# Kernel optimization log

Measured on AMD Instinct MI355X. Metric: run time of the kernel, lower is better.

The kernel has to match this reference:

```python
import jax, jax.numpy as jnp
import numpy as np

EMBED_DIM = 768
HEAD_SIZE = 64

def setup_inputs() -> dict:
    key = jax.random.key(0)
    k1, k2, k3, k4 = jax.random.split(key, 4)
    x = jax.random.normal(k1, (4, 4096, EMBED_DIM), dtype=jnp.float32)
    # nn.Linear(E, H, bias=False) weights, stored as [E, H] for y = x @ W
    scale = 1.0 / np.sqrt(EMBED_DIM)
    Wk = jax.random.uniform(k2, (EMBED_DIM, HEAD_SIZE), jnp.float32, -scale, scale)
    Wq = jax.random.uniform(k3, (EMBED_DIM, HEAD_SIZE), jnp.float32, -scale, scale)
    Wv = jax.random.uniform(k4, (EMBED_DIM, HEAD_SIZE), jnp.float32, -scale, scale)
    return {"x": x, "Wk": Wk, "Wq": Wq, "Wv": Wv}

def reference(x, Wk, Wq, Wv):
    # x: [B, S, E]
    E = x.shape[2]
    K = jnp.einsum("bse,eh->bsh", x, Wk)  # [B, S, H]
    Q = jnp.einsum("bse,eh->bsh", x, Wq)
    V = jnp.einsum("bse,eh->bsh", x, Wv)
    # NOTE: original scales by embedding_dim**0.5, not head_size**0.5
    A = jnp.einsum("bqh,bkh->bqk", Q, K) / jnp.sqrt(jnp.asarray(E, x.dtype))
    A = jax.nn.softmax(A, axis=-1)
    # dropout is inference-mode identity
    return jnp.einsum("bqk,bkh->bqh", A, V)
```

## Files before the change

### kernel.cpp

```cpp
#include <hip/hip_runtime.h>

typedef __attribute__((ext_vector_type(8))) short short8;
typedef __attribute__((ext_vector_type(4))) short short4v;
typedef __attribute__((ext_vector_type(4))) float float4v;
typedef __attribute__((ext_vector_type(2))) int int2v;

__device__ __forceinline__ short f2bf(float f) {
    union { float f; unsigned u; } v; v.f = f;
    return (short)((v.u + 0x7fffu + ((v.u >> 16) & 1u)) >> 16);
}
__device__ __forceinline__ int pack2(float a, float b) {
    union { float f; unsigned u; } x, y; x.f = a; y.f = b;
    return (int)(((x.u + 0x8000u) >> 16) | ((y.u + 0x8000u) & 0xFFFF0000u));
}

__device__ __forceinline__ float fast_exp2(float x) {
#if __has_builtin(__builtin_amdgcn_exp2f)
    return __builtin_amdgcn_exp2f(x);
#else
    return exp2f(x);
#endif
}

__global__ void wtrans_kernel(const float* __restrict__ Wk, const float* __restrict__ Wq,
                              const float* __restrict__ Wv, short* __restrict__ Wt3T) {
    int idx = blockIdx.x * 256 + threadIdx.x;
    int p = idx / 12288;
    int rem = idx - p * 12288;
    int kstep = rem / 512;
    int r2 = rem - kstep * 512;
    int lane = r2 >> 3, i = r2 & 7;
    int quad = lane >> 4, l16 = lane & 15;
    int j = p >> 2, nt = p & 3;
    int n = nt * 16 + l16;
    int k = kstep * 32 + quad * 8 + i;
    const float* W = (j == 0) ? Wq : (j == 1 ? Wk : Wv);
    float scale = (j == 0) ? 0.05205877f : 1.0f;
    Wt3T[idx] = f2bf(W[k * 64 + n] * scale);
}

__global__ __launch_bounds__(256, 3) void proj_kernel(
    const float* __restrict__ x, const short* __restrict__ Wt3T,
    short* __restrict__ Qs, short* __restrict__ Kb, short* __restrict__ Vtr)
{
    __shared__ alignas(16) short As[24 * 512];
    const int tid = threadIdx.x;
    const int wave = tid >> 6, lane = tid & 63, quad = lane >> 4, l16 = lane & 15;
    const int m0 = blockIdx.x * 16;
    const int p0 = wave * 3;

    {
        const int r = tid >> 4, c16 = tid & 15;
        const float* xp = x + (size_t)(m0 + r) * 768 + c16 * 4;
        float4 v[12];
#pragma unroll
        for (int ch = 0; ch < 12; ++ch) v[ch] = *(const float4*)(xp + ch * 64);
#pragma unroll
        for (int ch = 0; ch < 12; ++ch) {
            const int cb = c16 * 4 + ch * 64;
            const int sidx = (cb >> 5) * 512 + ((((cb >> 3) & 3) * 16 + r) << 3) + (cb & 7);
            *(int2v*)&As[sidx] = (int2v){pack2(v[ch].x, v[ch].y), pack2(v[ch].z, v[ch].w)};
        }
    }
    __syncthreads();

    const short* wp0 = Wt3T + (size_t)(p0 + 0) * 12288 + lane * 8;
    const short* wp1 = Wt3T + (size_t)(p0 + 1) * 12288 + lane * 8;
    const short* wp2 = Wt3T + (size_t)(p0 + 2) * 12288 + lane * 8;

    float4v acc0 = (float4v){0.f, 0.f, 0.f, 0.f};
    float4v acc1 = acc0, acc2 = acc0;

#pragma unroll
    for (int it = 0; it < 24; ++it) {
        short8 a = *(const short8*)&As[it * 512 + lane * 8];
        short8 w0 = *(const short8*)(wp0 + it * 512);
        short8 w1 = *(const short8*)(wp1 + it * 512);
        short8 w2 = *(const short8*)(wp2 + it * 512);
        acc0 = __builtin_amdgcn_mfma_f32_16x16x32_bf16(a, w0, acc0, 0, 0, 0);
        acc1 = __builtin_amdgcn_mfma_f32_16x16x32_bf16(a, w1, acc1, 0, 0, 0);
        acc2 = __builtin_amdgcn_mfma_f32_16x16x32_bf16(a, w2, acc2, 0, 0, 0);
    }

    float4v accs[3] = {acc0, acc1, acc2};
#pragma unroll
    for (int t = 0; t < 3; ++t) {
        const int p = p0 + t, j = p >> 2, nt = p & 3;
        if (j < 2) {
            short* dst = (j == 0) ? Qs : Kb;
#pragma unroll
            for (int r = 0; r < 4; ++r)
                dst[(size_t)(m0 + quad * 4 + r) * 64 + nt * 16 + l16] = f2bf(accs[t][r]);
        }
    }
    __syncthreads();
    short* sm = As;
#pragma unroll
    for (int t = 0; t < 3; ++t) {
        const int p = p0 + t, nt = p & 3;
        if ((p >> 2) == 2)
#pragma unroll
            for (int r = 0; r < 4; ++r)
                sm[(quad * 4 + r) * 72 + nt * 16 + l16] = f2bf(accs[t][r]);
    }
    __syncthreads();
    {
        const int h = tid >> 2, si = (tid & 3) * 4;
        const int b = m0 >> 12, s0 = m0 & 4095;
        short4v tmp;
#pragma unroll
        for (int i = 0; i < 4; ++i) tmp[i] = sm[(si + i) * 72 + h];
        *(short4v*)(Vtr + (size_t)(b * 64 + h) * 4096 + s0 + si) = tmp;
    }
}

__global__ __launch_bounds__(256, 4) void attn_kernel(
    const short* __restrict__ Qs, const short* __restrict__ Kb, const short* __restrict__ Vt,
    float* __restrict__ out, float* __restrict__ Lsum, int kv_len)
{
    __shared__ alignas(16) short Kl[64 * 72];
    __shared__ alignas(16) short Vl[64 * 72];
    __shared__ alignas(16) short Pl[4 * 32 * 72];

    const int tid = threadIdx.x;
    const int wave = tid >> 6, lane = tid & 63, quad = lane >> 4, l16 = lane & 15;
    const int qt = blockIdx.x, b = blockIdx.y, sp = blockIdx.z;
    const int q0 = qt * 128;
    const int bS = b * 4096;
    const int kv0 = sp * kv_len;

    short8 qa[2][2];
#pragma unroll
    for (int mt = 0; mt < 2; ++mt)
#pragma unroll
        for (int ks = 0; ks < 2; ++ks)
            qa[mt][ks] = *(const short8*)(Qs + (size_t)(bS + q0 + wave * 32 + mt * 16 + l16) * 64 + ks * 32 + quad * 8);

    float4v o[2][4];
    float rs[2][4];
#pragma unroll
    for (int mt = 0; mt < 2; ++mt)
#pragma unroll
        for (int nt = 0; nt < 4; ++nt) o[mt][nt] = (float4v){0.f, 0.f, 0.f, 0.f};
#pragma unroll
    for (int mt = 0; mt < 2; ++mt)
#pragma unroll
        for (int r = 0; r < 4; ++r) rs[mt][r] = 0.f;

    const int sr = tid >> 2, sc = (tid & 3) * 16;
    short* plw = &Pl[wave * 2304];

    for (int kt = 0; kt < kv_len; kt += 64) {
        const int kvg = kv0 + kt;
        __syncthreads();
        {
            const short* src = Kb + (size_t)(bS + kvg + sr) * 64 + sc;
            *(short8*)&Kl[sr * 72 + sc]     = *(const short8*)src;
            *(short8*)&Kl[sr * 72 + sc + 8] = *(const short8*)(src + 8);
            const short* vs = Vt + (size_t)(b * 64 + sr) * 4096 + kvg + sc;
            *(short8*)&Vl[sr * 72 + sc]     = *(const short8*)vs;
            *(short8*)&Vl[sr * 72 + sc + 8] = *(const short8*)(vs + 8);
        }
        __syncthreads();

        float4v s[2][4];
#pragma unroll
        for (int nt = 0; nt < 4; ++nt) {
            short8 b0 = *(const short8*)&Kl[(nt * 16 + l16) * 72 + quad * 8];
            short8 b1 = *(const short8*)&Kl[(nt * 16 + l16) * 72 + 32 + quad * 8];
#pragma unroll
            for (int mt = 0; mt < 2; ++mt) {
                float4v a0 = (float4v){0.f, 0.f, 0.f, 0.f};
                a0 = __builtin_amdgcn_mfma_f32_16x16x32_bf16(qa[mt][0], b0, a0, 0, 0, 0);
                a0 = __builtin_amdgcn_mfma_f32_16x16x32_bf16(qa[mt][1], b1, a0, 0, 0, 0);
                s[mt][nt] = a0;
            }
        }

#pragma unroll
        for (int mt = 0; mt < 2; ++mt)
#pragma unroll
            for (int nt = 0; nt < 4; ++nt)
#pragma unroll
                for (int r = 0; r < 4; ++r) {
                    float p = fast_exp2(s[mt][nt][r]);
                    rs[mt][r] += p;
                    plw[(mt * 16 + quad * 4 + r) * 72 + nt * 16 + l16] =
                        (short)((__float_as_uint(p) + 0x8000u) >> 16);
                }

#pragma unroll
        for (int ks = 0; ks < 2; ++ks) {
            short8 bf[4];
#pragma unroll
            for (int nt = 0; nt < 4; ++nt)
                bf[nt] = *(const short8*)&Vl[(nt * 16 + l16) * 72 + ks * 32 + quad * 8];
#pragma unroll
            for (int mt = 0; mt < 2; ++mt) {
                short8 af = *(const short8*)&plw[(mt * 16 + l16) * 72 + ks * 32 + quad * 8];
#pragma unroll
                for (int nt = 0; nt < 4; ++nt)
                    o[mt][nt] = __builtin_amdgcn_mfma_f32_16x16x32_bf16(af, bf[nt], o[mt][nt], 0, 0, 0);
            }
        }
    }

#pragma unroll
    for (int mt = 0; mt < 2; ++mt)
#pragma unroll
        for (int r = 0; r < 4; ++r) {
#pragma unroll
            for (int off = 8; off >= 1; off >>= 1)
                rs[mt][r] += __shfl_xor(rs[mt][r], off);
        }

#pragma unroll
    for (int mt = 0; mt < 2; ++mt) {
#pragma unroll
        for (int nt = 0; nt < 4; ++nt)
#pragma unroll
            for (int r = 0; r < 4; ++r) {
                int qb = q0 + wave * 32 + mt * 16 + quad * 4 + r;
                atomicAdd(&out[(size_t)(bS + qb) * 64 + nt * 16 + l16], o[mt][nt][r]);
            }
        if (l16 == 0) {
#pragma unroll
            for (int r = 0; r < 4; ++r) {
                int qb = q0 + wave * 32 + mt * 16 + quad * 4 + r;
                atomicAdd(&Lsum[bS + qb], rs[mt][r]);
            }
        }
    }
}

__global__ void normalize_kernel(float* __restrict__ out, const float* __restrict__ Lsum) {
    int idx = blockIdx.x * 256 + threadIdx.x;
    out[idx] /= Lsum[idx >> 6];
}

extern "C" void kernel_launch(void* const* d_in, const int* in_sizes, int n_in,
                              void* d_out, int out_size, void* d_ws, size_t ws_size,
                              hipStream_t stream) {
    const float* x  = (const float*)d_in[0];
    const float* Wk = (const float*)d_in[1];
    const float* Wq = (const float*)d_in[2];
    const float* Wv = (const float*)d_in[3];
    float* out = (float*)d_out;

    char* w = (char*)d_ws;
    size_t off = 0;
    auto take = [&](size_t bytes) -> void* {
        void* p = w + off;
        off = (off + bytes + 255) & ~(size_t)255;
        return p;
    };
    short* Qs   = (short*)take((size_t)16384 * 64 * 2);
    short* Kb   = (short*)take((size_t)16384 * 64 * 2);
    short* Vt   = (short*)take((size_t)16384 * 64 * 2);
    short* Wt3  = (short*)take((size_t)3 * 64 * 768 * 2);
    float* Lsum = (float*)take((size_t)16384 * 4);

    hipMemsetAsync(out, 0, (size_t)out_size * sizeof(float), stream);
    hipMemsetAsync(Lsum, 0, (size_t)16384 * 4, stream);

    wtrans_kernel<<<576, 256, 0, stream>>>(Wk, Wq, Wv, Wt3);
    proj_kernel<<<1024, 256, 0, stream>>>(x, Wt3, Qs, Kb, Vt);
    const int nsplit = 8;
    dim3 ag(32, 4, nsplit);
    attn_kernel<<<ag, 256, 0, stream>>>(Qs, Kb, Vt, out, Lsum, 4096 / nsplit);
    normalize_kernel<<<4096, 256, 0, stream>>>(out, Lsum);
}
```

Before: 153.0 us.

## Prefetch K/V tiles into registers and transpose QK MFMA for packed P stores

Global loads of the next K/V tile are issued into registers right after the LDS barrier, so they overlap with the current tile's compute instead of stalling at the start of each iteration. The QK^T MFMA swaps its operands, which makes each lane hold four consecutive kv columns for one query row. Exp and bf16 packing then happen inline and are written to LDS as one 8-byte store instead of scalar short stores. Row sums shrink to one scalar per tile, with a cheaper cross-quad shuffle and fewer Lsum atomics. The trade-off is extra registers for the prefetch buffers, which may hurt occupancy under launch_bounds(256,4).

```diff
diff --git a/kernel.cpp b/kernel.cpp
--- a/kernel.cpp
+++ b/kernel.cpp
@@ -131,63 +131,56 @@
 
     short8 qa[2][2];
 #pragma unroll
-    for (int mt = 0; mt < 2; ++mt)
+    for (int qt2 = 0; qt2 < 2; ++qt2)
 #pragma unroll
         for (int ks = 0; ks < 2; ++ks)
-            qa[mt][ks] = *(const short8*)(Qs + (size_t)(bS + q0 + wave * 32 + mt * 16 + l16) * 64 + ks * 32 + quad * 8);
+            qa[qt2][ks] = *(const short8*)(Qs + (size_t)(bS + q0 + wave * 32 + qt2 * 16 + l16) * 64 + ks * 32 + quad * 8);
 
     float4v o[2][4];
-    float rs[2][4];
-#pragma unroll
-    for (int mt = 0; mt < 2; ++mt)
-#pragma unroll
-        for (int nt = 0; nt < 4; ++nt) o[mt][nt] = (float4v){0.f, 0.f, 0.f, 0.f};
-#pragma unroll
-    for (int mt = 0; mt < 2; ++mt)
-#pragma unroll
-        for (int r = 0; r < 4; ++r) rs[mt][r] = 0.f;
+    float rs[2] = {0.f, 0.f};
+#pragma unroll
+    for (int qt2 = 0; qt2 < 2; ++qt2)
+#pragma unroll
+        for (int nt = 0; nt < 4; ++nt) o[qt2][nt] = (float4v){0.f, 0.f, 0.f, 0.f};
 
     const int sr = tid >> 2, sc = (tid & 3) * 16;
     short* plw = &Pl[wave * 2304];
 
+    const short* kp = Kb + (size_t)(bS + kv0 + sr) * 64 + sc;
+    const short* vp = Vt + (size_t)(b * 64 + sr) * 4096 + kv0 + sc;
+    short8 kr0 = *(const short8*)kp,       kr1 = *(const short8*)(kp + 8);
+    short8 vr0 = *(const short8*)vp,       vr1 = *(const short8*)(vp + 8);
+
     for (int kt = 0; kt < kv_len; kt += 64) {
-        const int kvg = kv0 + kt;
         __syncthreads();
-        {
-            const short* src = Kb + (size_t)(bS + kvg + sr) * 64 + sc;
-            *(short8*)&Kl[sr * 72 + sc]     = *(const short8*)src;
-            *(short8*)&Kl[sr * 72 + sc + 8] = *(const short8*)(src + 8);
-            const short* vs = Vt + (size_t)(b * 64 + sr) * 4096 + kvg + sc;
-            *(short8*)&Vl[sr * 72 + sc]     = *(const short8*)vs;
-            *(short8*)&Vl[sr * 72 + sc + 8] = *(const short8*)(vs + 8);
-        }
+        *(short8*)&Kl[sr * 72 + sc]     = kr0;
+        *(short8*)&Kl[sr * 72 + sc + 8] = kr1;
+        *(short8*)&Vl[sr * 72 + sc]     = vr0;
+        *(short8*)&Vl[sr * 72 + sc + 8] = vr1;
         __syncthreads();
 
-        float4v s[2][4];
-#pragma unroll
-        for (int nt = 0; nt < 4; ++nt) {
-            short8 b0 = *(const short8*)&Kl[(nt * 16 + l16) * 72 + quad * 8];
-            short8 b1 = *(const short8*)&Kl[(nt * 16 + l16) * 72 + 32 + quad * 8];
-#pragma unroll
-            for (int mt = 0; mt < 2; ++mt) {
+        if (kt + 64 < kv_len) {
+            kp += 64 * 64; vp += 64;
+            kr0 = *(const short8*)kp; kr1 = *(const short8*)(kp + 8);
+            vr0 = *(const short8*)vp; vr1 = *(const short8*)(vp + 8);
+        }
+
+#pragma unroll
+        for (int kvt = 0; kvt < 4; ++kvt) {
+            short8 ka0 = *(const short8*)&Kl[(kvt * 16 + l16) * 72 + quad * 8];
+            short8 ka1 = *(const short8*)&Kl[(kvt * 16 + l16) * 72 + 32 + quad * 8];
+#pragma unroll
+            for (int qt2 = 0; qt2 < 2; ++qt2) {
                 float4v a0 = (float4v){0.f, 0.f, 0.f, 0.f};
-                a0 = __builtin_amdgcn_mfma_f32_16x16x32_bf16(qa[mt][0], b0, a0, 0, 0, 0);
-                a0 = __builtin_amdgcn_mfma_f32_16x16x32_bf16(qa[mt][1], b1, a0, 0, 0, 0);
-                s[mt][nt] = a0;
+                a0 = __builtin_amdgcn_mfma_f32_16x16x32_bf16(ka0, qa[qt2][0], a0, 0, 0, 0);
+                a0 = __builtin_amdgcn_mfma_f32_16x16x32_bf16(ka1, qa[qt2][1], a0, 0, 0, 0);
+                float p0 = fast_exp2(a0[0]), p1 = fast_exp2(a0[1]);
+                float p2 = fast_exp2(a0[2]), p3 = fast_exp2(a0[3]);
+                rs[qt2] += (p0 + p1) + (p2 + p3);
+                *(int2v*)&plw[(qt2 * 16 + l16) * 72 + kvt * 16 + quad * 4] =
+                    (int2v){pack2(p0, p1), pack2(p2, p3)};
             }
         }
-
-#pragma unroll
-        for (int mt = 0; mt < 2; ++mt)
-#pragma unroll
-            for (int nt = 0; nt < 4; ++nt)
-#pragma unroll
-                for (int r = 0; r < 4; ++r) {
-                    float p = fast_exp2(s[mt][nt][r]);
-                    rs[mt][r] += p;
-                    plw[(mt * 16 + quad * 4 + r) * 72 + nt * 16 + l16] =
-                        (short)((__float_as_uint(p) + 0x8000u) >> 16);
-                }
 
 #pragma unroll
         for (int ks = 0; ks < 2; ++ks) {
@@ -196,40 +189,32 @@
             for (int nt = 0; nt < 4; ++nt)
                 bf[nt] = *(const short8*)&Vl[(nt * 16 + l16) * 72 + ks * 32 + quad * 8];
 #pragma unroll
-            for (int mt = 0; mt < 2; ++mt) {
-                short8 af = *(const short8*)&plw[(mt * 16 + l16) * 72 + ks * 32 + quad * 8];
+            for (int qt2 = 0; qt2 < 2; ++qt2) {
+                short8 af = *(const short8*)&plw[(qt2 * 16 + l16) * 72 + ks * 32 + quad * 8];
 #pragma unroll
                 for (int nt = 0; nt < 4; ++nt)
-                    o[mt][nt] = __builtin_amdgcn_mfma_f32_16x16x32_bf16(af, bf[nt], o[mt][nt], 0, 0, 0);
+                    o[qt2][nt] = __builtin_amdgcn_mfma_f32_16x16x32_bf16(af, bf[nt], o[qt2][nt], 0, 0, 0);
             }
         }
     }
 
 #pragma unroll
-    for (int mt = 0; mt < 2; ++mt)
-#pragma unroll
-        for (int r = 0; r < 4; ++r) {
-#pragma unroll
-            for (int off = 8; off >= 1; off >>= 1)
-                rs[mt][r] += __shfl_xor(rs[mt][r], off);
-        }
-
-#pragma unroll
-    for (int mt = 0; mt < 2; ++mt) {
+    for (int qt2 = 0; qt2 < 2; ++qt2) {
+        rs[qt2] += __shfl_xor(rs[qt2], 16);
+        rs[qt2] += __shfl_xor(rs[qt2], 32);
+    }
+
+#pragma unroll
+    for (int qt2 = 0; qt2 < 2; ++qt2) {
 #pragma unroll
         for (int nt = 0; nt < 4; ++nt)
 #pragma unroll
             for (int r = 0; r < 4; ++r) {
-                int qb = q0 + wave * 32 + mt * 16 + quad * 4 + r;
-                atomicAdd(&out[(size_t)(bS + qb) * 64 + nt * 16 + l16], o[mt][nt][r]);
+                int qb = q0 + wave * 32 + qt2 * 16 + quad * 4 + r;
+                atomicAdd(&out[(size_t)(bS + qb) * 64 + nt * 16 + l16], o[qt2][nt][r]);
             }
-        if (l16 == 0) {
-#pragma unroll
-            for (int r = 0; r < 4; ++r) {
-                int qb = q0 + wave * 32 + mt * 16 + quad * 4 + r;
-                atomicAdd(&Lsum[bS + qb], rs[mt][r]);
-            }
-        }
+        if (quad == 0)
+            atomicAdd(&Lsum[bS + q0 + wave * 32 + qt2 * 16 + l16], rs[qt2]);
     }
 }
 
```

After: 146.2 us. 4.5% less time.
